# Kernel tuning notes

Hardware: AMD Instinct MI355X
Metric: run time of the kernel (lower is better)

## Reference

```python
import jax, jax.numpy as jnp
import numpy as np

B = 128          # persons in the batch
V = 300          # visits per person (< MAX_VISITS so all kept)
MAX_VISITS = 510 # 512 - 2, hard-coded in the module
D = 256          # embedding_dim * n_heads
VOCAB = 50000
MAX_DAYS = 365


def setup_inputs() -> dict:
    key = jax.random.key(0)
    k_codes, k_times, k_emb = jax.random.split(key, 3)

    total_visits = B * V  # 38400
    v = np.arange(total_visits)
    codes_per_visit = 8 + (v % 8)                      # 8..15 codes per visit
    code_to_visit = np.repeat(v, codes_per_visit).astype(np.int32)  # sorted segment ids (sum_indices)
    total_codes = code_to_visit.shape[0]               # 441600
    visit_person = (v // V).astype(np.int32)
    visit_slot = (MAX_VISITS - V + (v % V)).astype(np.int32)  # right-aligned slots

    all_codes = jax.random.randint(k_codes, (total_codes,), 0, VOCAB, dtype=jnp.int32)
    times = jax.random.uniform(k_times, (total_visits,), dtype=jnp.float32) * (MAX_DAYS - 1)
    concept_emb = jax.random.normal(k_emb, (VOCAB, D), dtype=jnp.float32)
    pad_embedding = jnp.zeros((D,), dtype=jnp.float32)  # torch.nn.Parameter(torch.zeros(D))
    # ((1/10000) ** (1/D)) ** range(D//2)
    timescales = jnp.asarray(((1.0 / 10000.0) ** (1.0 / D)) ** np.arange(D // 2), dtype=jnp.float32)

    return {
        "all_codes": all_codes,
        "code_to_visit": jnp.asarray(code_to_visit),
        "visit_person": jnp.asarray(visit_person),
        "visit_slot": jnp.asarray(visit_slot),
        "times": times,
        "concept_emb": concept_emb,
        "pad_embedding": pad_embedding,
        "timescales": timescales,
    }


def reference(all_codes, code_to_visit, visit_person, visit_slot, times,
              concept_emb, pad_embedding, timescales):
    total_visits = visit_person.shape[0]
    d = concept_emb.shape[1]

    # concept-embedding gather: [total_codes, D]
    embedded_raw = concept_emb[all_codes]

    # per-visit segment sum (index_add_): [total_visits, D]
    summed = jax.ops.segment_sum(embedded_raw, code_to_visit,
                                 num_segments=total_visits,
                                 indices_are_sorted=True)

    # padded tensor initialised with pad_embedding, then right-aligned scatter of visits
    base = jnp.zeros((B, MAX_VISITS, d), dtype=summed.dtype) + pad_embedding
    reshaped = base.at[visit_person, visit_slot].set(summed)

    # sinusoidal time embedding: cat(sin(t*ts), cos(t*ts))
    t = jnp.clip(times, 0.0, MAX_DAYS - 1)
    ang = t[:, None] * timescales[None, :]                       # [total_visits, D/2]
    temb_un = jnp.concatenate([jnp.sin(ang), jnp.cos(ang)], 1)   # [total_visits, D]
    time_embedding = jnp.zeros((B, MAX_VISITS, d), dtype=summed.dtype)
    time_embedding = time_embedding.at[visit_person, visit_slot].set(temb_un)

    return reshaped + time_embedding
```

## Files before the change

kernel.cpp:

```cpp
#include <hip/hip_runtime.h>

#define MAXV 510
#define D4 64

typedef float floatx4 __attribute__((ext_vector_type(4)));

__global__ __launch_bounds__(256) void build_maps(
    const int* __restrict__ c2v,
    const int* __restrict__ person,
    const int* __restrict__ slot,
    int* __restrict__ inv,
    int* __restrict__ off,
    int total_codes, int total_visits)
{
    int v = blockIdx.x * blockDim.x + threadIdx.x;
    if (v >= total_visits) return;
    inv[person[v] * MAXV + slot[v]] = v;
    int lo = 0, hi = total_codes;
    while (lo < hi) {
        int m = (lo + hi) >> 1;
        if (c2v[m] < v) lo = m + 1; else hi = m;
    }
    off[v] = lo;
    if (v == 0) off[total_visits] = total_codes;
}

__global__ __launch_bounds__(256) void fused_kernel(
    const int* __restrict__ all_codes,
    const float* __restrict__ times,
    const floatx4* __restrict__ emb,
    const floatx4* __restrict__ pad,
    const floatx4* __restrict__ tsc,
    const int* __restrict__ inv,
    const int* __restrict__ off,
    floatx4* __restrict__ out,
    int nslots)
{
    const int tid = threadIdx.x;
    const int w = tid >> 6;
    const int lane = tid & 63;
    const int slot_id = blockIdx.x * 4 + w;
    if (slot_id >= nslots) return;

    const int v = inv[slot_id];
    if (v < 0) {
        __builtin_nontemporal_store(pad[lane], &out[slot_id * D4 + lane]);
        return;
    }

    const int lo = off[v];
    const int hi = off[v + 1];
    const int cnt = hi - lo;

    floatx4 acc = (floatx4)(0.f);
    for (int base = 0; base < cnt; base += 64) {
        const int n = min(cnt - base, 64);
        const int mycode = (lane < n) ? all_codes[lo + base + lane]
                                      : all_codes[lo];
        for (int j = 0; j < n; j += 4) {
            const int i1 = min(j + 1, n - 1);
            const int i2 = min(j + 2, n - 1);
            const int i3 = min(j + 3, n - 1);
            const int c0 = __shfl(mycode, j);
            const int c1 = __shfl(mycode, i1);
            const int c2 = __shfl(mycode, i2);
            const int c3 = __shfl(mycode, i3);
            const floatx4 e0 = emb[c0 * D4 + lane];
            const floatx4 e1 = emb[c1 * D4 + lane];
            const floatx4 e2 = emb[c2 * D4 + lane];
            const floatx4 e3 = emb[c3 * D4 + lane];
            acc += e0;
            if (j + 1 < n) acc += e1;
            if (j + 2 < n) acc += e2;
            if (j + 3 < n) acc += e3;
        }
    }

    float t = times[v];
    t = fminf(fmaxf(t, 0.f), 364.f);
    const floatx4 ts = tsc[lane & 31];
    floatx4 te;
    if (lane < 32) {
        te.x = sinf(t * ts.x); te.y = sinf(t * ts.y);
        te.z = sinf(t * ts.z); te.w = sinf(t * ts.w);
    } else {
        te.x = cosf(t * ts.x); te.y = cosf(t * ts.y);
        te.z = cosf(t * ts.z); te.w = cosf(t * ts.w);
    }

    __builtin_nontemporal_store(acc + te, &out[slot_id * D4 + lane]);
}

extern "C" void kernel_launch(void* const* d_in, const int* in_sizes, int n_in,
                              void* d_out, int out_size, void* d_ws, size_t ws_size,
                              hipStream_t stream) {
    const int*   all_codes = (const int*)d_in[0];
    const int*   c2v       = (const int*)d_in[1];
    const int*   person    = (const int*)d_in[2];
    const int*   slot      = (const int*)d_in[3];
    const float* times     = (const float*)d_in[4];
    const float* emb       = (const float*)d_in[5];
    const float* pad       = (const float*)d_in[6];
    const float* tsc       = (const float*)d_in[7];

    const int total_codes  = in_sizes[0];
    const int total_visits = in_sizes[2];
    const int nslots       = out_size / 256;

    int* inv = (int*)d_ws;
    int* off = inv + nslots;

    (void)hipMemsetAsync(inv, 0xFF, (size_t)nslots * sizeof(int), stream);

    build_maps<<<(total_visits + 255) / 256, 256, 0, stream>>>(
        c2v, person, slot, inv, off, total_codes, total_visits);

    fused_kernel<<<(nslots + 3) / 4, 256, 0, stream>>>(
        all_codes, times, (const floatx4*)emb, (const floatx4*)pad,
        (const floatx4*)tsc, inv, off, (floatx4*)d_out, nslots);
}
```

Measured before the change: 175.3 us.

## Gather embeddings from a bf16 copy of the table built each call

Each call converts the fp32 concept embedding table to bf16 in workspace, then gathers half-width rows and accumulates them in fp32, with the time embedding used as the starting accumulator. This is meant to halve the bytes moved by the random gather. The cost is a full read of the 51 MB table plus a 25 MB write on every call, and a loss of precision in the embeddings. A simpler fp32 fallback kernel runs when the workspace is too small.

```diff
diff --git a/kernel.cpp b/kernel.cpp
--- a/kernel.cpp
+++ b/kernel.cpp
@@ -4,6 +4,32 @@
 #define D4 64
 
 typedef float floatx4 __attribute__((ext_vector_type(4)));
+
+__device__ __forceinline__ unsigned int pack2_bf16_rne(float a, float b) {
+    unsigned int ua = __builtin_bit_cast(unsigned int, a);
+    unsigned int ub = __builtin_bit_cast(unsigned int, b);
+    ua = (ua + 0x7FFFu + ((ua >> 16) & 1u)) >> 16;
+    ub = (ub + 0x7FFFu + ((ub >> 16) & 1u)) >> 16;
+    return ua | (ub << 16);
+}
+
+__device__ __forceinline__ float bf16_to_f32(unsigned short u) {
+    return __builtin_bit_cast(float, (unsigned int)u << 16);
+}
+
+__global__ __launch_bounds__(256) void convert_bf16(
+    const float4* __restrict__ in, uint4* __restrict__ out, int npairs) {
+    int i = blockIdx.x * blockDim.x + threadIdx.x;
+    if (i >= npairs) return;
+    const float4 a = in[2 * i];
+    const float4 b = in[2 * i + 1];
+    uint4 r;
+    r.x = pack2_bf16_rne(a.x, a.y);
+    r.y = pack2_bf16_rne(a.z, a.w);
+    r.z = pack2_bf16_rne(b.x, b.y);
+    r.w = pack2_bf16_rne(b.z, b.w);
+    out[i] = r;
+}
 
 __global__ __launch_bounds__(256) void build_maps(
     const int* __restrict__ c2v,
@@ -25,7 +51,75 @@
     if (v == 0) off[total_visits] = total_codes;
 }
 
-__global__ __launch_bounds__(256) void fused_kernel(
+__global__ __launch_bounds__(256) void fused_bf16(
+    const int* __restrict__ all_codes,
+    const float* __restrict__ times,
+    const ushort4* __restrict__ embh,
+    const floatx4* __restrict__ pad,
+    const floatx4* __restrict__ tsc,
+    const int* __restrict__ inv,
+    const int* __restrict__ off,
+    floatx4* __restrict__ out,
+    int nslots)
+{
+    const int tid = threadIdx.x;
+    const int w = tid >> 6;
+    const int lane = tid & 63;
+    const int slot_id = blockIdx.x * 4 + w;
+    if (slot_id >= nslots) return;
+
+    const int v = inv[slot_id];
+    if (v < 0) {
+        __builtin_nontemporal_store(pad[lane], &out[slot_id * D4 + lane]);
+        return;
+    }
+
+    const int lo = off[v];
+    const int hi = off[v + 1];
+    const int cnt = hi - lo;
+
+    float t = times[v];
+    t = fminf(fmaxf(t, 0.f), 364.f);
+    const floatx4 ts = tsc[lane & 31];
+    floatx4 acc;
+    if (lane < 32) {
+        acc.x = sinf(t * ts.x); acc.y = sinf(t * ts.y);
+        acc.z = sinf(t * ts.z); acc.w = sinf(t * ts.w);
+    } else {
+        acc.x = cosf(t * ts.x); acc.y = cosf(t * ts.y);
+        acc.z = cosf(t * ts.z); acc.w = cosf(t * ts.w);
+    }
+
+    for (int base = 0; base < cnt; base += 64) {
+        const int n = min(cnt - base, 64);
+        const int mycode = all_codes[lo + base + min(lane, n - 1)];
+        for (int j = 0; j < n; j += 4) {
+            const int i1 = min(j + 1, n - 1);
+            const int i2 = min(j + 2, n - 1);
+            const int i3 = min(j + 3, n - 1);
+            const int c0 = __shfl(mycode, j);
+            const int c1 = __shfl(mycode, i1);
+            const int c2 = __shfl(mycode, i2);
+            const int c3 = __shfl(mycode, i3);
+            const ushort4 e0 = embh[c0 * D4 + lane];
+            const ushort4 e1 = embh[c1 * D4 + lane];
+            const ushort4 e2 = embh[c2 * D4 + lane];
+            const ushort4 e3 = embh[c3 * D4 + lane];
+            acc.x += bf16_to_f32(e0.x); acc.y += bf16_to_f32(e0.y);
+            acc.z += bf16_to_f32(e0.z); acc.w += bf16_to_f32(e0.w);
+            if (j + 1 < n) { acc.x += bf16_to_f32(e1.x); acc.y += bf16_to_f32(e1.y);
+                             acc.z += bf16_to_f32(e1.z); acc.w += bf16_to_f32(e1.w); }
+            if (j + 2 < n) { acc.x += bf16_to_f32(e2.x); acc.y += bf16_to_f32(e2.y);
+                             acc.z += bf16_to_f32(e2.z); acc.w += bf16_to_f32(e2.w); }
+            if (j + 3 < n) { acc.x += bf16_to_f32(e3.x); acc.y += bf16_to_f32(e3.y);
+                             acc.z += bf16_to_f32(e3.z); acc.w += bf16_to_f32(e3.w); }
+        }
+    }
+
+    __builtin_nontemporal_store(acc, &out[slot_id * D4 + lane]);
+}
+
+__global__ __launch_bounds__(256) void fused_f32(
     const int* __restrict__ all_codes,
     const float* __restrict__ times,
     const floatx4* __restrict__ emb,
@@ -47,48 +141,26 @@
         __builtin_nontemporal_store(pad[lane], &out[slot_id * D4 + lane]);
         return;
     }
-
     const int lo = off[v];
     const int hi = off[v + 1];
     const int cnt = hi - lo;
 
-    floatx4 acc = (floatx4)(0.f);
-    for (int base = 0; base < cnt; base += 64) {
-        const int n = min(cnt - base, 64);
-        const int mycode = (lane < n) ? all_codes[lo + base + lane]
-                                      : all_codes[lo];
-        for (int j = 0; j < n; j += 4) {
-            const int i1 = min(j + 1, n - 1);
-            const int i2 = min(j + 2, n - 1);
-            const int i3 = min(j + 3, n - 1);
-            const int c0 = __shfl(mycode, j);
-            const int c1 = __shfl(mycode, i1);
-            const int c2 = __shfl(mycode, i2);
-            const int c3 = __shfl(mycode, i3);
-            const floatx4 e0 = emb[c0 * D4 + lane];
-            const floatx4 e1 = emb[c1 * D4 + lane];
-            const floatx4 e2 = emb[c2 * D4 + lane];
-            const floatx4 e3 = emb[c3 * D4 + lane];
-            acc += e0;
-            if (j + 1 < n) acc += e1;
-            if (j + 2 < n) acc += e2;
-            if (j + 3 < n) acc += e3;
-        }
-    }
-
     float t = times[v];
     t = fminf(fmaxf(t, 0.f), 364.f);
     const floatx4 ts = tsc[lane & 31];
-    floatx4 te;
+    floatx4 acc;
     if (lane < 32) {
-        te.x = sinf(t * ts.x); te.y = sinf(t * ts.y);
-        te.z = sinf(t * ts.z); te.w = sinf(t * ts.w);
+        acc.x = sinf(t * ts.x); acc.y = sinf(t * ts.y);
+        acc.z = sinf(t * ts.z); acc.w = sinf(t * ts.w);
     } else {
-        te.x = cosf(t * ts.x); te.y = cosf(t * ts.y);
-        te.z = cosf(t * ts.z); te.w = cosf(t * ts.w);
-    }
-
-    __builtin_nontemporal_store(acc + te, &out[slot_id * D4 + lane]);
+        acc.x = cosf(t * ts.x); acc.y = cosf(t * ts.y);
+        acc.z = cosf(t * ts.z); acc.w = cosf(t * ts.w);
+    }
+    for (int i = lo; i < hi; ++i) {
+        const int c = all_codes[i];
+        acc += emb[(size_t)c * D4 + lane];
+    }
+    __builtin_nontemporal_store(acc, &out[slot_id * D4 + lane]);
 }
 
 extern "C" void kernel_launch(void* const* d_in, const int* in_sizes, int n_in,
@@ -105,17 +177,31 @@
 
     const int total_codes  = in_sizes[0];
     const int total_visits = in_sizes[2];
+    const int emb_elems    = in_sizes[5];
     const int nslots       = out_size / 256;
 
-    int* inv = (int*)d_ws;
+    char* ws = (char*)d_ws;
+    int* inv = (int*)ws;
     int* off = inv + nslots;
+    size_t head = ((size_t)(nslots + total_visits + 1) * sizeof(int) + 255) & ~(size_t)255;
+    unsigned short* embh = (unsigned short*)(ws + head);
+    const size_t needed = head + (size_t)emb_elems * sizeof(unsigned short);
 
     (void)hipMemsetAsync(inv, 0xFF, (size_t)nslots * sizeof(int), stream);
 
     build_maps<<<(total_visits + 255) / 256, 256, 0, stream>>>(
         c2v, person, slot, inv, off, total_codes, total_visits);
 
-    fused_kernel<<<(nslots + 3) / 4, 256, 0, stream>>>(
-        all_codes, times, (const floatx4*)emb, (const floatx4*)pad,
-        (const floatx4*)tsc, inv, off, (floatx4*)d_out, nslots);
-}
+    if (ws_size >= needed) {
+        const int npairs = emb_elems / 8;
+        convert_bf16<<<(npairs + 255) / 256, 256, 0, stream>>>(
+            (const float4*)emb, (uint4*)embh, npairs);
+        fused_bf16<<<(nslots + 3) / 4, 256, 0, stream>>>(
+            all_codes, times, (const ushort4*)embh, (const floatx4*)pad,
+            (const floatx4*)tsc, inv, off, (floatx4*)d_out, nslots);
+    } else {
+        fused_f32<<<(nslots + 3) / 4, 256, 0, stream>>>(
+            all_codes, times, (const floatx4*)emb, (const floatx4*)pad,
+            (const floatx4*)tsc, inv, off, (floatx4*)d_out, nslots);
+    }
+}
```

Result: faster. 165.6 us (-5.5%).
